# Kernel tuning notes

Hardware: AMD Instinct MI355X
Metric: run time of the kernel (lower is better)

The kernel has to match this reference:

```python
import jax, jax.numpy as jnp
import numpy as np

FEATURE_DIM = 256
HEADS = 8


def setup_inputs() -> dict:
    key = jax.random.key(0)
    ks = jax.random.split(key, 9)
    d, h = FEATURE_DIM, HEADS
    b, n = 4, 4096
    s_in = 1.0 / np.sqrt(d)
    s_out = 1.0 / np.sqrt(d * h)
    return {
        "x": jax.random.normal(ks[0], (b, n, d), dtype=jnp.float32),
        "Wq": jax.random.uniform(ks[1], (d, d * h), jnp.float32, -s_in, s_in),
        "bq": jax.random.uniform(ks[2], (d * h,), jnp.float32, -s_in, s_in),
        "Wk": jax.random.uniform(ks[3], (d, d * h), jnp.float32, -s_in, s_in),
        "bk": jax.random.uniform(ks[4], (d * h,), jnp.float32, -s_in, s_in),
        "Wv": jax.random.uniform(ks[5], (d, d * h), jnp.float32, -s_in, s_in),
        "bv": jax.random.uniform(ks[6], (d * h,), jnp.float32, -s_in, s_in),
        "Wo": jax.random.uniform(ks[7], (d * h, d), jnp.float32, -s_out, s_out),
        "bo": jax.random.uniform(ks[8], (d,), jnp.float32, -s_out, s_out),
    }


def reference(x, Wq, bq, Wk, bk, Wv, bv, Wo, bo):
    b, n, d = x.shape
    h = HEADS
    scale = d ** (-0.5)
    # projections: (b, n, h, d) -- note: NO head transpose, matching original
    q = (x @ Wq + bq).reshape(b, n, h, d)
    k = (x @ Wk + bk).reshape(b, n, h, d)
    v = (x @ Wv + bv).reshape(b, n, h, d)
    # attention is head-vs-head per token: (b, n, h, h)
    attn = jnp.einsum("bnhd,bngd->bnhg", q, k) * scale
    attn = jax.nn.softmax(attn, axis=-1)
    out = jnp.einsum("bnhg,bngd->bnhd", attn, v).reshape(b, n, h * d)
    return out @ Wo + bo
```

## Files before the change

### kernel.cpp

```cpp
#include <hip/hip_runtime.h>
#include <hip/hip_bf16.h>
#include <math.h>

typedef __bf16 bf16;
typedef __bf16 bf16x4 __attribute__((ext_vector_type(4)));
typedef __bf16 bf16x8 __attribute__((ext_vector_type(8)));
typedef float f32x4 __attribute__((ext_vector_type(4)));
typedef unsigned int u32;
typedef u32 __attribute__((address_space(1))) gu32;
typedef u32 __attribute__((address_space(3))) lu32;

#define TOK   16384
#define D_    256
#define HD    2048
#define VN    2048

#define GLDS16(g, l) __builtin_amdgcn_global_load_lds((gu32*)(g), (lu32*)(l), 16, 0, 0)
#define WAIT_VM(n)  __builtin_amdgcn_s_waitcnt(0x0F70 | (n))
#define WAIT_LGKM0  __builtin_amdgcn_s_waitcnt(0xC07F)
#define BAR() do { __builtin_amdgcn_s_barrier(); __builtin_amdgcn_sched_barrier(0); } while (0)

__device__ __forceinline__ void transpose_body(
    const void* __restrict__ src, bf16* __restrict__ dst, int R, int C,
    int tc, int tr, int f, int mode, float (*tile)[33])
{
    int lx = threadIdx.x & 31, ly = threadIdx.x >> 5;
    for (int i = 0; i < 4; i++) {
        int r = ly + i * 8;
        size_t idx = (size_t)(tr + r) * C + tc + lx;
        tile[r][lx] = f ? ((const float*)src)[idx] : (float)((const bf16*)src)[idx];
    }
    __syncthreads();
    for (int i = 0; i < 4; i++) {
        int r = ly + i * 8;
        int k = tr + lx;
        int n = tc + r;
        size_t di;
        if (mode == 1)
            di = (size_t)n * 2048 + ((k & 255) << 3) + (k >> 8);
        else if (mode == 2)
            di = (size_t)(4096 + ((n & 255) << 3) + (n >> 8)) * 256 + k;
        else if (mode == 3)
            di = (size_t)((((n & 255) >> 4) << 8) + ((n >> 8) << 4) + (n & 15)) * 256 + k;
        else if (mode == 4)
            di = (size_t)((((n & 255) >> 4) << 8) + 128 + ((n >> 8) << 4) + (n & 15)) * 256 + k;
        else
            di = (size_t)n * R + k;
        dst[di] = (bf16)tile[lx][r];
    }
}

__global__ __launch_bounds__(256) void prep(
    const void* __restrict__ x,
    const void* __restrict__ Wq, const void* __restrict__ bq,
    const void* __restrict__ Wk, const void* __restrict__ bk,
    const void* __restrict__ Wv, const void* __restrict__ bv,
    const void* __restrict__ Wo, const void* __restrict__ bo,
    bf16* __restrict__ xb, bf16* __restrict__ WTI, bf16* __restrict__ WoT,
    bf16* __restrict__ bqkv, bf16* __restrict__ bob)
{
    __shared__ float tile[32][33];
    __shared__ int sflag;
    int tid = threadIdx.x;
    if (tid == 0) sflag = 0;
    __syncthreads();
    {
        float v = fabsf((float)((const bf16*)x)[2 * tid]);
        if (!(v < 1e4f)) sflag = 1;
    }
    __syncthreads();
    int f = sflag;
    int b = blockIdx.x;

    if (b < 4096) {
        int i = b * 256 + tid;
        bf16x4 o;
        if (f) { f32x4 v = ((const f32x4*)x)[i]; for (int e = 0; e < 4; e++) o[e] = (bf16)v[e]; }
        else   { o = ((const bf16x4*)x)[i]; }
        ((bf16x4*)xb)[i] = o;
    } else if (b < 4121) {
        int i = (b - 4096) * 256 + tid;
        if (i < 6400) {
            const void* src; bf16* dst = bqkv; int off, woff;
            if (i < 2048) {
                src = bq; off = i;
                int d = off & 255, h = off >> 8;
                woff = ((d >> 4) << 8) + (h << 4) + (d & 15);
            } else if (i < 4096) {
                src = bk; off = i - 2048;
                int d = off & 255, h = off >> 8;
                woff = ((d >> 4) << 8) + 128 + (h << 4) + (d & 15);
            } else if (i < 6144) {
                src = bv; off = i - 4096;
                woff = 4096 + ((off & 255) << 3) + (off >> 8);
            } else {
                src = bo; dst = bob; off = i - 6144; woff = off;
            }
            float v = f ? ((const float*)src)[off] : (float)((const bf16*)src)[off];
            dst[woff] = (bf16)v;
        }
        __syncthreads();
    } else if (b < 5657) {
        int idx = b - 4121;
        int tx = idx & 63, rest = idx >> 6;
        int ty = rest & 7, tz = rest >> 3;
        const void* src = (tz == 0) ? Wq : (tz == 1) ? Wk : Wv;
        int mode = (tz == 0) ? 3 : (tz == 1) ? 4 : 2;
        transpose_body(src, WTI, 256, 2048, tx * 32, ty * 32, f, mode, tile);
    } else {
        int idx = b - 5657;
        int tx = idx & 7, ty = idx >> 3;
        transpose_body(Wo, WoT, 2048, 256, tx * 32, ty * 32, f, 1, tile);
    }
}

__global__ __launch_bounds__(256) void v_proj(
    const bf16* __restrict__ X, const bf16* __restrict__ WT,
    const bf16* __restrict__ bI, bf16* __restrict__ vout)
{
    __shared__ char smem[36864];
    bf16* As = (bf16*)smem;
    bf16* Bs = (bf16*)(smem + 16384);
    int m0 = blockIdx.y * 128, n0 = blockIdx.x * 128;
    int tid = threadIdx.x, wave = tid >> 6, lane = tid & 63;
    int wm = (wave >> 1) * 64, wn = (wave & 1) * 64;
    int mrow = lane & 15, quad = lane >> 4;
    int lrow8 = lane >> 3, lslot = lane & 7;

    f32x4 acc[4][4] = {};
    for (int k0 = 0; k0 < D_; k0 += 64) {
        __syncthreads();
        for (int i = 0; i < 4; i++) {
            int rbase = wave * 32 + i * 8;
            int row = rbase + lrow8;
            int gc = lslot ^ (row & 7);
            GLDS16(&X[(size_t)(m0 + row) * D_ + k0 + gc * 8], &As[rbase * 64]);
            GLDS16(&WT[(size_t)(n0 + row) * D_ + k0 + gc * 8], &Bs[rbase * 64]);
        }
        __syncthreads();
        for (int kk = 0; kk < 64; kk += 32) {
            int slot = (((kk >> 3) + quad) ^ (mrow & 7)) * 8;
            bf16x8 af[4], bfv[4];
            for (int mt = 0; mt < 4; mt++)
                af[mt] = *(const bf16x8*)&As[(wm + mt * 16 + mrow) * 64 + slot];
            for (int nt = 0; nt < 4; nt++)
                bfv[nt] = *(const bf16x8*)&Bs[(wn + nt * 16 + mrow) * 64 + slot];
            for (int mt = 0; mt < 4; mt++)
                for (int nt = 0; nt < 4; nt++)
                    acc[mt][nt] = __builtin_amdgcn_mfma_f32_16x16x32_bf16(
                        bfv[nt], af[mt], acc[mt][nt], 0, 0, 0);
        }
    }

    __syncthreads();
    bf16* ep = (bf16*)smem + wave * (64 * 72);
    for (int mt = 0; mt < 4; mt++) {
        for (int nt = 0; nt < 4; nt++) {
            int col = n0 + wn + nt * 16 + quad * 4;
            bf16x4 bb = *(const bf16x4*)&bI[col];
            bf16x4 o;
            for (int r = 0; r < 4; r++) o[r] = (bf16)(acc[mt][nt][r] + (float)bb[r]);
            *(bf16x4*)&ep[(mt * 16 + mrow) * 72 + nt * 16 + quad * 4] = o;
        }
    }
    __syncthreads();
    for (int i = 0; i < 8; i++) {
        int r = i * 8 + (lane >> 3);
        int cb = (lane & 7) * 8;
        bf16x8 val = *(const bf16x8*)&ep[r * 72 + cb];
        *(bf16x8*)&vout[(size_t)(m0 + wm + r) * VN + n0 + wn + cb] = val;
    }
}

__global__ __launch_bounds__(512, 2) void qk_score(
    const bf16* __restrict__ X, const bf16* __restrict__ WTI,
    const bf16* __restrict__ bI, float* __restrict__ P)
{
    __shared__ bf16 Ws[3][64 * 256];
    __shared__ bf16 qkh[64 * 256];
    int tid = threadIdx.x, wave = tid >> 6, lane = tid & 63;
    int mrow = lane & 15, quad = lane >> 4;
    int wm3 = (wave >> 2) * 32, wn3 = (wave & 3) * 16;
    int h = lane >> 3, g = lane & 7;
    int t0 = blockIdx.x * 64;

#pragma unroll
    for (int i = 0; i < 4; i++) {
        int row = (i * 8 + wave) * 2 + (lane >> 5);
        int sl = lane & 31;
        int gc = (sl & 24) | ((sl & 7) ^ (row & 7));
        GLDS16(&X[(size_t)(t0 + row) * 256 + gc * 8], &Ws[2][(i * 8 + wave) * 512]);
    }
    WAIT_VM(0);
    BAR();
#pragma unroll
    for (int i = 0; i < 4; i++) {
        int row = (i * 8 + wave) * 2 + (lane >> 5);
        int sl = lane & 31;
        int gc = (sl & 24) | ((sl & 7) ^ (row & 7));
        GLDS16(&WTI[(size_t)row * 256 + gc * 8], &Ws[0][(i * 8 + wave) * 512]);
    }
#pragma unroll
    for (int i = 0; i < 4; i++) {
        int row = (i * 8 + wave) * 2 + (lane >> 5);
        int sl = lane & 31;
        int gc = (sl & 24) | ((sl & 7) ^ (row & 7));
        GLDS16(&WTI[(size_t)(64 + row) * 256 + gc * 8], &Ws[1][(i * 8 + wave) * 512]);
    }
    bf16x8 areg[2][8];
#pragma unroll
    for (int mt = 0; mt < 2; mt++)
#pragma unroll
        for (int ks = 0; ks < 8; ks++) {
            int arow = wm3 + mt * 16 + mrow;
            int sl = ks * 4 + quad;
            int ph = (sl & 24) | ((sl & 7) ^ (arow & 7));
            areg[mt][ks] = *(const bf16x8*)&Ws[2][arow * 256 + ph * 8];
        }
    WAIT_LGKM0;
    BAR();

    float S[8] = {};

    for (int s = 0; s < 64; s++) {
        int cur = s % 3;
        if (s == 63) { WAIT_VM(0); } else { WAIT_VM(4); }
        BAR();
        if (s <= 61) {
            int nb = (s + 2) % 3;
#pragma unroll
            for (int i = 0; i < 4; i++) {
                int row = (i * 8 + wave) * 2 + (lane >> 5);
                int sl = lane & 31;
                int gc = (sl & 24) | ((sl & 7) ^ (row & 7));
                GLDS16(&WTI[(size_t)((s + 2) * 64 + row) * 256 + gc * 8],
                       &Ws[nb][(i * 8 + wave) * 512]);
            }
        }

        int brow = wn3 + mrow;
        bf16x8 bv[8];
#pragma unroll
        for (int ks = 0; ks < 8; ks++) {
            int sl = ks * 4 + quad;
            int ph = (sl & 24) | ((sl & 7) ^ (brow & 7));
            bv[ks] = *(const bf16x8*)&Ws[cur][brow * 256 + ph * 8];
        }
        f32x4 acc0 = {}, acc1 = {};
#pragma unroll
        for (int ks = 0; ks < 8; ks++) {
            acc0 = __builtin_amdgcn_mfma_f32_16x16x32_bf16(bv[ks], areg[0][ks], acc0, 0, 0, 0);
            acc1 = __builtin_amdgcn_mfma_f32_16x16x32_bf16(bv[ks], areg[1][ks], acc1, 0, 0, 0);
        }

        int sub = s & 3, qk = sub >> 1;
        int hh = (sub & 1) * 4 + (wn3 >> 4);
        bf16x4 bb = *(const bf16x4*)&bI[s * 64 + wn3 + quad * 4];
#pragma unroll
        for (int mt = 0; mt < 2; mt++) {
            int t = wm3 + mt * 16 + mrow;
            f32x4 a = mt ? acc1 : acc0;
            bf16x4 o;
#pragma unroll
            for (int r = 0; r < 4; r++) o[r] = (bf16)(a[r] + (float)bb[r]);
            int bo = ((qk << 8) + (hh << 5) + (quad << 3)) ^ ((t & 7) << 4);
            *(bf16x4*)((char*)qkh + t * 512 + bo) = o;
        }

        if ((s & 3) == 3) {
            WAIT_LGKM0;
            BAR();
#pragma unroll
            for (int ti = 0; ti < 8; ti++) {
                int t = wave * 8 + ti;
                int swz = (t & 7) << 4;
                const char* base = (const char*)qkh + t * 512;
                bf16x8 q0 = *(const bf16x8*)(base + (((h << 5)) ^ swz));
                bf16x8 q1 = *(const bf16x8*)(base + (((h << 5) + 16) ^ swz));
                bf16x8 k0 = *(const bf16x8*)(base + ((256 + (g << 5)) ^ swz));
                bf16x8 k1 = *(const bf16x8*)(base + ((256 + (g << 5) + 16) ^ swz));
                float a = 0.f;
#pragma unroll
                for (int e = 0; e < 8; e++)
                    a += (float)q0[e] * (float)k0[e] + (float)q1[e] * (float)k1[e];
                S[ti] += a;
            }
            WAIT_LGKM0;
        }
    }

#pragma unroll
    for (int ti = 0; ti < 8; ti++) {
        int t = t0 + wave * 8 + ti;
        float sc = S[ti] * 0.0625f;
        float m = sc;
        for (int off = 1; off < 8; off <<= 1) m = fmaxf(m, __shfl_xor(m, off, 8));
        float p = __expf(sc - m);
        float sum = p;
        for (int off = 1; off < 8; off <<= 1) sum += __shfl_xor(sum, off, 8);
        P[(size_t)t * 64 + lane] = p / sum;
    }
}

__global__ __launch_bounds__(256) void out_fused(
    const bf16* __restrict__ vb, const bf16* __restrict__ WoT,
    const float* __restrict__ P, const bf16* __restrict__ bob,
    float* __restrict__ outp)
{
    __shared__ bf16 Bs[2][256 * 64];
    __shared__ bf16 Vs[2][32 * 64];
    int m0 = blockIdx.x * 32;
    int tid = threadIdx.x, wave = tid >> 6, lane = tid & 63;
    int wm = (wave >> 1) * 16, wn = (wave & 1) * 128;
    int mrow = lane & 15, quad = lane >> 4;
    int t = wm + mrow, ts = t & 7;
    int sl8 = lane >> 3, sl = lane & 7;

    float Pv[64];
    {
        const float* pr = P + (size_t)(m0 + t) * 64;
#pragma unroll
        for (int j = 0; j < 16; j++) {
            f32x4 v4 = *(const f32x4*)&pr[j * 4];
            Pv[4 * j + 0] = v4[0]; Pv[4 * j + 1] = v4[1];
            Pv[4 * j + 2] = v4[2]; Pv[4 * j + 3] = v4[3];
        }
    }

    f32x4 acc[8] = {};
    {
        int tt = (wave << 3) + sl8;
        GLDS16(&vb[(size_t)(m0 + tt) * VN + ((sl ^ (tt & 7)) << 3)],
               &Vs[0][wave * 512]);
#pragma unroll
        for (int i = 0; i < 8; i++) {
            int n = (wave << 6) + (i << 3) + sl8;
            GLDS16(&WoT[(size_t)n * HD + ((sl ^ (n & 7)) << 3)],
                   &Bs[0][((wave << 6) + (i << 3)) << 6]);
        }
    }

    for (int c = 0; c < 32; c++) {
        __syncthreads();
        if (c < 31) {
            int cc = c + 1, bb = cc & 1;
            int tt = (wave << 3) + sl8;
            GLDS16(&vb[(size_t)(m0 + tt) * VN + cc * 64 + ((sl ^ (tt & 7)) << 3)],
                   &Vs[bb][wave * 512]);
#pragma unroll
            for (int i = 0; i < 8; i++) {
                int n = (wave << 6) + (i << 3) + sl8;
                GLDS16(&WoT[(size_t)n * HD + cc * 64 + ((sl ^ (n & 7)) << 3)],
                       &Bs[bb][((wave << 6) + (i << 3)) << 6]);
            }
        }
        const bf16* Vb = Vs[c & 1];
        const bf16* Bb = Bs[c & 1];

        bf16x8 vf0 = *(const bf16x8*)&Vb[(t << 6) + ((quad ^ ts) << 3)];
        bf16x8 vf1 = *(const bf16x8*)&Vb[(t << 6) + (((quad + 4) ^ ts) << 3)];
        float v0f[8], v1f[8];
#pragma unroll
        for (int e = 0; e < 8; e++) { v0f[e] = (float)vf0[e]; v1f[e] = (float)vf1[e]; }
        bf16x8 af0, af1;
#pragma unroll
        for (int hh = 0; hh < 8; hh++) {
            float a0 = 0.f, a1 = 0.f;
#pragma unroll
            for (int gg = 0; gg < 8; gg++) {
                a0 += Pv[hh * 8 + gg] * v0f[gg];
                a1 += Pv[hh * 8 + gg] * v1f[gg];
            }
            af0[hh] = (bf16)a0; af1[hh] = (bf16)a1;
        }
#pragma unroll
        for (int nt = 0; nt < 8; nt++) {
            bf16x8 bv = *(const bf16x8*)&Bb[(wn + nt * 16 + mrow) * 64
                            + ((quad ^ (mrow & 7)) << 3)];
            acc[nt] = __builtin_amdgcn_mfma_f32_16x16x32_bf16(bv, af0, acc[nt], 0, 0, 0);
        }
#pragma unroll
        for (int nt = 0; nt < 8; nt++) {
            bf16x8 bv = *(const bf16x8*)&Bb[(wn + nt * 16 + mrow) * 64
                            + (((4 + quad) ^ (mrow & 7)) << 3)];
            acc[nt] = __builtin_amdgcn_mfma_f32_16x16x32_bf16(bv, af1, acc[nt], 0, 0, 0);
        }
    }

    int row = m0 + wm + mrow;
#pragma unroll
    for (int nt = 0; nt < 8; nt++) {
        int col = wn + nt * 16 + quad * 4;
        bf16x4 bb = *(const bf16x4*)&bob[col];
        f32x4 o;
        for (int r = 0; r < 4; r++) o[r] = acc[nt][r] + (float)bb[r];
        *(f32x4*)&outp[(size_t)row * D_ + col] = o;
    }
}

extern "C" void kernel_launch(void* const* d_in, const int* in_sizes, int n_in,
                              void* d_out, int out_size, void* d_ws, size_t ws_size,
                              hipStream_t stream)
{
    const void* x  = d_in[0];
    const void* Wq = d_in[1];
    const void* bq = d_in[2];
    const void* Wk = d_in[3];
    const void* bk = d_in[4];
    const void* Wv = d_in[5];
    const void* bv = d_in[6];
    const void* Wo = d_in[7];
    const void* bo = d_in[8];
    float* out = (float*)d_out;

    char* ws = (char*)d_ws;
    bf16*  vbuf = (bf16*)ws;
    bf16*  WTI  = (bf16*)(ws + 67108864);
    bf16*  WoT  = (bf16*)(ws + 70254592);
    bf16*  xb   = (bf16*)(ws + 71303168);
    bf16*  bqkv = (bf16*)(ws + 79691776);
    bf16*  bob  = (bf16*)(ws + 79704064);
    float* Pbuf = (float*)(ws + 79704576);

    prep<<<6169, 256, 0, stream>>>(x, Wq, bq, Wk, bk, Wv, bv, Wo, bo,
                                   xb, WTI, WoT, bqkv, bob);
    qk_score<<<256, 512, 0, stream>>>(xb, WTI, bqkv, Pbuf);
    v_proj<<<dim3(16, 128), 256, 0, stream>>>(xb, WTI + 4096 * 256, bqkv + 4096, vbuf);
    out_fused<<<512, 256, 0, stream>>>(vbuf, WoT, Pbuf, bob, out);
}
```

Before: 270.3 us.

## Load QK weights directly to registers and double-buffer qkh score staging

The qk_score kernel no longer stages the fused Q/K weight tiles through a triple-buffered LDS ring. Each wave now loads its B fragments straight from global memory into two register buffers, prefetching two steps ahead. The per-token head-score partials use a double-buffered qkh in LDS, so each group's dot products are spread across the next group's four MFMA steps. This cuts the per-step barrier to one per four steps and shrinks LDS, which may raise occupancy. In exchange each wave does uncoalesced-ish global reads of weights, relying on cache, and register pressure rises.

```diff
diff --git a/kernel.cpp b/kernel.cpp
--- a/kernel.cpp
+++ b/kernel.cpp
@@ -176,8 +176,7 @@
     const bf16* __restrict__ X, const bf16* __restrict__ WTI,
     const bf16* __restrict__ bI, float* __restrict__ P)
 {
-    __shared__ bf16 Ws[3][64 * 256];
-    __shared__ bf16 qkh[64 * 256];
+    __shared__ bf16 qkh[2][64 * 256];
     int tid = threadIdx.x, wave = tid >> 6, lane = tid & 63;
     int mrow = lane & 15, quad = lane >> 4;
     int wm3 = (wave >> 2) * 32, wn3 = (wave & 3) * 16;
@@ -189,24 +188,10 @@
         int row = (i * 8 + wave) * 2 + (lane >> 5);
         int sl = lane & 31;
         int gc = (sl & 24) | ((sl & 7) ^ (row & 7));
-        GLDS16(&X[(size_t)(t0 + row) * 256 + gc * 8], &Ws[2][(i * 8 + wave) * 512]);
+        GLDS16(&X[(size_t)(t0 + row) * 256 + gc * 8], &qkh[0][(i * 8 + wave) * 512]);
     }
     WAIT_VM(0);
     BAR();
-#pragma unroll
-    for (int i = 0; i < 4; i++) {
-        int row = (i * 8 + wave) * 2 + (lane >> 5);
-        int sl = lane & 31;
-        int gc = (sl & 24) | ((sl & 7) ^ (row & 7));
-        GLDS16(&WTI[(size_t)row * 256 + gc * 8], &Ws[0][(i * 8 + wave) * 512]);
-    }
-#pragma unroll
-    for (int i = 0; i < 4; i++) {
-        int row = (i * 8 + wave) * 2 + (lane >> 5);
-        int sl = lane & 31;
-        int gc = (sl & 24) | ((sl & 7) ^ (row & 7));
-        GLDS16(&WTI[(size_t)(64 + row) * 256 + gc * 8], &Ws[1][(i * 8 + wave) * 512]);
-    }
     bf16x8 areg[2][8];
 #pragma unroll
     for (int mt = 0; mt < 2; mt++)
@@ -215,77 +200,93 @@
             int arow = wm3 + mt * 16 + mrow;
             int sl = ks * 4 + quad;
             int ph = (sl & 24) | ((sl & 7) ^ (arow & 7));
-            areg[mt][ks] = *(const bf16x8*)&Ws[2][arow * 256 + ph * 8];
-        }
+            areg[mt][ks] = *(const bf16x8*)&qkh[0][arow * 256 + ph * 8];
+        }
+    const bf16* wbase = WTI + (size_t)(wn3 + mrow) * 256 + quad * 8;
+    bf16x8 bvA[8], bvB[8];
+#define QK_LOAD(BV, SS) {                                                      \
+        const bf16* wp_ = wbase + (size_t)(SS) * 16384;                        \
+        _Pragma("unroll")                                                      \
+        for (int ks = 0; ks < 8; ks++) BV[ks] = *(const bf16x8*)(wp_ + ks * 32); }
+    QK_LOAD(bvA, 0)
+    QK_LOAD(bvB, 1)
     WAIT_LGKM0;
     BAR();
 
     float S[8] = {};
 
-    for (int s = 0; s < 64; s++) {
-        int cur = s % 3;
-        if (s == 63) { WAIT_VM(0); } else { WAIT_VM(4); }
+#define QK_BODY(SUB, BV) {                                                     \
+        f32x4 acc0 = {}, acc1 = {};                                            \
+        _Pragma("unroll")                                                      \
+        for (int ks = 0; ks < 8; ks++) {                                       \
+            acc0 = __builtin_amdgcn_mfma_f32_16x16x32_bf16(BV[ks], areg[0][ks], acc0, 0, 0, 0); \
+            acc1 = __builtin_amdgcn_mfma_f32_16x16x32_bf16(BV[ks], areg[1][ks], acc1, 0, 0, 0); \
+        }                                                                      \
+        int s_ = db4 * 4 + (SUB);                                              \
+        int hh = ((SUB) & 1) * 4 + (wave & 3);                                 \
+        bf16x4 bb = *(const bf16x4*)&bI[s_ * 64 + wn3 + quad * 4];             \
+        char* wqk = (char*)qkh[db4 & 1];                                       \
+        _Pragma("unroll")                                                      \
+        for (int mt = 0; mt < 2; mt++) {                                       \
+            int t = wm3 + mt * 16 + mrow;                                      \
+            f32x4 a = mt ? acc1 : acc0;                                        \
+            bf16x4 o;                                                          \
+            for (int r = 0; r < 4; r++) o[r] = (bf16)(a[r] + (float)bb[r]);    \
+            int bo = ((((SUB) >> 1) << 8) + (hh << 5) + (quad << 3)) ^ ((t & 7) << 4); \
+            *(bf16x4*)(wqk + t * 512 + bo) = o;                                \
+        }                                                                      \
+        if (db4 > 0) {                                                         \
+            const char* sb = (const char*)qkh[(db4 & 1) ^ 1];                  \
+            _Pragma("unroll")                                                  \
+            for (int u = 0; u < 2; u++) {                                      \
+                int tt = (SUB) * 2 + u;                                        \
+                int t = wave * 8 + tt;                                         \
+                int swz = (t & 7) << 4;                                        \
+                const char* base = sb + t * 512;                               \
+                bf16x8 q0 = *(const bf16x8*)(base + ((h << 5) ^ swz));         \
+                bf16x8 q1 = *(const bf16x8*)(base + (((h << 5) + 16) ^ swz));  \
+                bf16x8 k0 = *(const bf16x8*)(base + ((256 + (g << 5)) ^ swz)); \
+                bf16x8 k1 = *(const bf16x8*)(base + ((256 + (g << 5) + 16) ^ swz)); \
+                float a = 0.f;                                                 \
+                _Pragma("unroll")                                              \
+                for (int e = 0; e < 8; e++)                                    \
+                    a += (float)q0[e] * (float)k0[e] + (float)q1[e] * (float)k1[e]; \
+                S[tt] += a;                                                    \
+            }                                                                  \
+        }                                                                      \
+    }
+
+    for (int db4 = 0; db4 < 16; db4++) {
+        QK_BODY(0, bvA)
+        QK_LOAD(bvA, db4 * 4 + 2)
+        QK_BODY(1, bvB)
+        QK_LOAD(bvB, db4 * 4 + 3)
+        QK_BODY(2, bvA)
+        if (db4 < 15) QK_LOAD(bvA, db4 * 4 + 4)
+        QK_BODY(3, bvB)
+        if (db4 < 15) QK_LOAD(bvB, db4 * 4 + 5)
+        WAIT_LGKM0;
         BAR();
-        if (s <= 61) {
-            int nb = (s + 2) % 3;
-#pragma unroll
-            for (int i = 0; i < 4; i++) {
-                int row = (i * 8 + wave) * 2 + (lane >> 5);
-                int sl = lane & 31;
-                int gc = (sl & 24) | ((sl & 7) ^ (row & 7));
-                GLDS16(&WTI[(size_t)((s + 2) * 64 + row) * 256 + gc * 8],
-                       &Ws[nb][(i * 8 + wave) * 512]);
-            }
-        }
-
-        int brow = wn3 + mrow;
-        bf16x8 bv[8];
-#pragma unroll
-        for (int ks = 0; ks < 8; ks++) {
-            int sl = ks * 4 + quad;
-            int ph = (sl & 24) | ((sl & 7) ^ (brow & 7));
-            bv[ks] = *(const bf16x8*)&Ws[cur][brow * 256 + ph * 8];
-        }
-        f32x4 acc0 = {}, acc1 = {};
-#pragma unroll
-        for (int ks = 0; ks < 8; ks++) {
-            acc0 = __builtin_amdgcn_mfma_f32_16x16x32_bf16(bv[ks], areg[0][ks], acc0, 0, 0, 0);
-            acc1 = __builtin_amdgcn_mfma_f32_16x16x32_bf16(bv[ks], areg[1][ks], acc1, 0, 0, 0);
-        }
-
-        int sub = s & 3, qk = sub >> 1;
-        int hh = (sub & 1) * 4 + (wn3 >> 4);
-        bf16x4 bb = *(const bf16x4*)&bI[s * 64 + wn3 + quad * 4];
-#pragma unroll
-        for (int mt = 0; mt < 2; mt++) {
-            int t = wm3 + mt * 16 + mrow;
-            f32x4 a = mt ? acc1 : acc0;
-            bf16x4 o;
-#pragma unroll
-            for (int r = 0; r < 4; r++) o[r] = (bf16)(a[r] + (float)bb[r]);
-            int bo = ((qk << 8) + (hh << 5) + (quad << 3)) ^ ((t & 7) << 4);
-            *(bf16x4*)((char*)qkh + t * 512 + bo) = o;
-        }
-
-        if ((s & 3) == 3) {
-            WAIT_LGKM0;
-            BAR();
-#pragma unroll
-            for (int ti = 0; ti < 8; ti++) {
-                int t = wave * 8 + ti;
-                int swz = (t & 7) << 4;
-                const char* base = (const char*)qkh + t * 512;
-                bf16x8 q0 = *(const bf16x8*)(base + (((h << 5)) ^ swz));
-                bf16x8 q1 = *(const bf16x8*)(base + (((h << 5) + 16) ^ swz));
-                bf16x8 k0 = *(const bf16x8*)(base + ((256 + (g << 5)) ^ swz));
-                bf16x8 k1 = *(const bf16x8*)(base + ((256 + (g << 5) + 16) ^ swz));
-                float a = 0.f;
-#pragma unroll
-                for (int e = 0; e < 8; e++)
-                    a += (float)q0[e] * (float)k0[e] + (float)q1[e] * (float)k1[e];
-                S[ti] += a;
-            }
-            WAIT_LGKM0;
+    }
+#undef QK_BODY
+#undef QK_LOAD
+
+    {
+        const char* sb = (const char*)qkh[1];
+#pragma unroll
+        for (int tt = 0; tt < 8; tt++) {
+            int t = wave * 8 + tt;
+            int swz = (t & 7) << 4;
+            const char* base = sb + t * 512;
+            bf16x8 q0 = *(const bf16x8*)(base + ((h << 5) ^ swz));
+            bf16x8 q1 = *(const bf16x8*)(base + (((h << 5) + 16) ^ swz));
+            bf16x8 k0 = *(const bf16x8*)(base + ((256 + (g << 5)) ^ swz));
+            bf16x8 k1 = *(const bf16x8*)(base + ((256 + (g << 5) + 16) ^ swz));
+            float a = 0.f;
+#pragma unroll
+            for (int e = 0; e < 8; e++)
+                a += (float)q0[e] * (float)k0[e] + (float)q1[e] * (float)k1[e];
+            S[tt] += a;
         }
     }
 
```

Result: slower. 339.7 us (+25.7%).

## Halve qk_score token tile and drop triple-buffered weight pipeline for occupancy

Applied to the files above, without the earlier changes.

The qk_score kernel now processes 32 tokens per block instead of 64, launching 512 blocks, and replaces the three-stage async weight buffer with a single LDS buffer loaded synchronously each step. This cuts LDS use and registers so up to four blocks per CU can be resident, aiming to hide latency through occupancy rather than software pipelining. It also adds an extra XOR swizzle on the qkh scratch layout to avoid bank conflicts in the reduction reads. The trade-off is that weight tiles are now reloaded by twice as many blocks, and each step waits on its own load with two barriers instead of overlapping it.

```diff
diff --git a/kernel.cpp b/kernel.cpp
--- a/kernel.cpp
+++ b/kernel.cpp
@@ -16,7 +16,6 @@
 #define VN    2048
 
 #define GLDS16(g, l) __builtin_amdgcn_global_load_lds((gu32*)(g), (lu32*)(l), 16, 0, 0)
-#define WAIT_VM(n)  __builtin_amdgcn_s_waitcnt(0x0F70 | (n))
 #define WAIT_LGKM0  __builtin_amdgcn_s_waitcnt(0xC07F)
 #define BAR() do { __builtin_amdgcn_s_barrier(); __builtin_amdgcn_sched_barrier(0); } while (0)
 
@@ -172,71 +171,51 @@
     }
 }
 
-__global__ __launch_bounds__(512, 2) void qk_score(
+__global__ __launch_bounds__(512, 4) void qk_score(
     const bf16* __restrict__ X, const bf16* __restrict__ WTI,
     const bf16* __restrict__ bI, float* __restrict__ P)
 {
-    __shared__ bf16 Ws[3][64 * 256];
-    __shared__ bf16 qkh[64 * 256];
+    __shared__ bf16 Ws[64 * 256];
+    __shared__ bf16 qkh[32 * 256];
     int tid = threadIdx.x, wave = tid >> 6, lane = tid & 63;
     int mrow = lane & 15, quad = lane >> 4;
-    int wm3 = (wave >> 2) * 32, wn3 = (wave & 3) * 16;
+    int wm3 = (wave >> 2) * 16, wn3 = (wave & 3) * 16;
     int h = lane >> 3, g = lane & 7;
-    int t0 = blockIdx.x * 64;
-
-#pragma unroll
-    for (int i = 0; i < 4; i++) {
-        int row = (i * 8 + wave) * 2 + (lane >> 5);
+    int hx = (h & 4) << 2, gx = (g & 4) << 2;
+    int t0 = blockIdx.x * 32;
+
+#pragma unroll
+    for (int i = 0; i < 2; i++) {
+        int row = i * 16 + wave * 2 + (lane >> 5);
         int sl = lane & 31;
         int gc = (sl & 24) | ((sl & 7) ^ (row & 7));
-        GLDS16(&X[(size_t)(t0 + row) * 256 + gc * 8], &Ws[2][(i * 8 + wave) * 512]);
-    }
-    WAIT_VM(0);
-    BAR();
-#pragma unroll
-    for (int i = 0; i < 4; i++) {
-        int row = (i * 8 + wave) * 2 + (lane >> 5);
-        int sl = lane & 31;
-        int gc = (sl & 24) | ((sl & 7) ^ (row & 7));
-        GLDS16(&WTI[(size_t)row * 256 + gc * 8], &Ws[0][(i * 8 + wave) * 512]);
-    }
-#pragma unroll
-    for (int i = 0; i < 4; i++) {
-        int row = (i * 8 + wave) * 2 + (lane >> 5);
-        int sl = lane & 31;
-        int gc = (sl & 24) | ((sl & 7) ^ (row & 7));
-        GLDS16(&WTI[(size_t)(64 + row) * 256 + gc * 8], &Ws[1][(i * 8 + wave) * 512]);
-    }
-    bf16x8 areg[2][8];
-#pragma unroll
-    for (int mt = 0; mt < 2; mt++)
-#pragma unroll
-        for (int ks = 0; ks < 8; ks++) {
-            int arow = wm3 + mt * 16 + mrow;
-            int sl = ks * 4 + quad;
-            int ph = (sl & 24) | ((sl & 7) ^ (arow & 7));
-            areg[mt][ks] = *(const bf16x8*)&Ws[2][arow * 256 + ph * 8];
-        }
+        GLDS16(&X[(size_t)(t0 + row) * 256 + gc * 8], &qkh[(i * 16 + wave * 2) * 256]);
+    }
+    __syncthreads();
+    bf16x8 areg[8];
+#pragma unroll
+    for (int ks = 0; ks < 8; ks++) {
+        int arow = wm3 + mrow;
+        int sl = ks * 4 + quad;
+        int ph = (sl & 24) | ((sl & 7) ^ (arow & 7));
+        areg[ks] = *(const bf16x8*)&qkh[arow * 256 + ph * 8];
+    }
     WAIT_LGKM0;
     BAR();
 
-    float S[8] = {};
+    float S[4] = {};
 
     for (int s = 0; s < 64; s++) {
-        int cur = s % 3;
-        if (s == 63) { WAIT_VM(0); } else { WAIT_VM(4); }
-        BAR();
-        if (s <= 61) {
-            int nb = (s + 2) % 3;
-#pragma unroll
-            for (int i = 0; i < 4; i++) {
-                int row = (i * 8 + wave) * 2 + (lane >> 5);
-                int sl = lane & 31;
-                int gc = (sl & 24) | ((sl & 7) ^ (row & 7));
-                GLDS16(&WTI[(size_t)((s + 2) * 64 + row) * 256 + gc * 8],
-                       &Ws[nb][(i * 8 + wave) * 512]);
-            }
-        }
+        __syncthreads();
+#pragma unroll
+        for (int i = 0; i < 4; i++) {
+            int row = (i * 8 + wave) * 2 + (lane >> 5);
+            int sl = lane & 31;
+            int gc = (sl & 24) | ((sl & 7) ^ (row & 7));
+            GLDS16(&WTI[(size_t)(s * 64 + row) * 256 + gc * 8],
+                   &Ws[(i * 8 + wave) * 512]);
+        }
+        __syncthreads();
 
         int brow = wn3 + mrow;
         bf16x8 bv[8];
@@ -244,54 +223,51 @@
         for (int ks = 0; ks < 8; ks++) {
             int sl = ks * 4 + quad;
             int ph = (sl & 24) | ((sl & 7) ^ (brow & 7));
-            bv[ks] = *(const bf16x8*)&Ws[cur][brow * 256 + ph * 8];
-        }
-        f32x4 acc0 = {}, acc1 = {};
-#pragma unroll
-        for (int ks = 0; ks < 8; ks++) {
-            acc0 = __builtin_amdgcn_mfma_f32_16x16x32_bf16(bv[ks], areg[0][ks], acc0, 0, 0, 0);
-            acc1 = __builtin_amdgcn_mfma_f32_16x16x32_bf16(bv[ks], areg[1][ks], acc1, 0, 0, 0);
-        }
+            bv[ks] = *(const bf16x8*)&Ws[brow * 256 + ph * 8];
+        }
+        f32x4 acc = {};
+#pragma unroll
+        for (int ks = 0; ks < 8; ks++)
+            acc = __builtin_amdgcn_mfma_f32_16x16x32_bf16(bv[ks], areg[ks], acc, 0, 0, 0);
 
         int sub = s & 3, qk = sub >> 1;
-        int hh = (sub & 1) * 4 + (wn3 >> 4);
+        int hh = (sub & 1) * 4 + (wave & 3);
         bf16x4 bb = *(const bf16x4*)&bI[s * 64 + wn3 + quad * 4];
-#pragma unroll
-        for (int mt = 0; mt < 2; mt++) {
-            int t = wm3 + mt * 16 + mrow;
-            f32x4 a = mt ? acc1 : acc0;
+        {
+            int t = wm3 + mrow;
             bf16x4 o;
 #pragma unroll
-            for (int r = 0; r < 4; r++) o[r] = (bf16)(a[r] + (float)bb[r]);
-            int bo = ((qk << 8) + (hh << 5) + (quad << 3)) ^ ((t & 7) << 4);
+            for (int r = 0; r < 4; r++) o[r] = (bf16)(acc[r] + (float)bb[r]);
+            int bo = (((qk << 8) + (hh << 5) + (quad << 3))
+                      ^ ((t & 7) << 4)) ^ ((sub & 1) << 4);
             *(bf16x4*)((char*)qkh + t * 512 + bo) = o;
         }
 
-        if ((s & 3) == 3) {
+        if (sub == 3) {
             WAIT_LGKM0;
             BAR();
 #pragma unroll
-            for (int ti = 0; ti < 8; ti++) {
-                int t = wave * 8 + ti;
+            for (int u = 0; u < 4; u++) {
+                int t = wave * 4 + u;
                 int swz = (t & 7) << 4;
                 const char* base = (const char*)qkh + t * 512;
-                bf16x8 q0 = *(const bf16x8*)(base + (((h << 5)) ^ swz));
-                bf16x8 q1 = *(const bf16x8*)(base + (((h << 5) + 16) ^ swz));
-                bf16x8 k0 = *(const bf16x8*)(base + ((256 + (g << 5)) ^ swz));
-                bf16x8 k1 = *(const bf16x8*)(base + ((256 + (g << 5) + 16) ^ swz));
+                bf16x8 q0 = *(const bf16x8*)(base + ((((h << 5)) ^ hx) ^ swz));
+                bf16x8 q1 = *(const bf16x8*)(base + ((((h << 5) + 16) ^ hx) ^ swz));
+                bf16x8 k0 = *(const bf16x8*)(base + (256 + ((((g << 5)) ^ gx) ^ swz)));
+                bf16x8 k1 = *(const bf16x8*)(base + (256 + ((((g << 5) + 16) ^ gx) ^ swz)));
                 float a = 0.f;
 #pragma unroll
                 for (int e = 0; e < 8; e++)
                     a += (float)q0[e] * (float)k0[e] + (float)q1[e] * (float)k1[e];
-                S[ti] += a;
+                S[u] += a;
             }
             WAIT_LGKM0;
         }
     }
 
 #pragma unroll
-    for (int ti = 0; ti < 8; ti++) {
-        int t = t0 + wave * 8 + ti;
+    for (int ti = 0; ti < 4; ti++) {
+        int t = t0 + wave * 4 + ti;
         float sc = S[ti] * 0.0625f;
         float m = sc;
         for (int off = 1; off < 8; off <<= 1) m = fmaxf(m, __shfl_xor(m, off, 8));
@@ -424,7 +400,7 @@
 
     prep<<<6169, 256, 0, stream>>>(x, Wq, bq, Wk, bk, Wv, bv, Wo, bo,
                                    xb, WTI, WoT, bqkv, bob);
-    qk_score<<<256, 512, 0, stream>>>(xb, WTI, bqkv, Pbuf);
+    qk_score<<<512, 512, 0, stream>>>(xb, WTI, bqkv, Pbuf);
     v_proj<<<dim3(16, 128), 256, 0, stream>>>(xb, WTI + 4096 * 256, bqkv + 4096, vbuf);
     out_fused<<<512, 256, 0, stream>>>(vbuf, WoT, Pbuf, bob, out);
 }
```

Result: faster. 264.5 us (-2.2%).
